# Kernel optimization log

Hardware: AMD Instinct MI355X
Metric: run time of the kernel (lower is better)

The kernel has to match this reference:

```python
import jax, jax.numpy as jnp
import numpy as np

DIM, HEADS, RANK = 768, 12, 64
HEAD_DIM = DIM // HEADS

def _xavier(key, shape):
    fan_in, fan_out = shape[1], shape[0]
    std = (2.0 / (fan_in + fan_out)) ** 0.5
    return std * jax.random.normal(key, shape, dtype=jnp.float32)

def setup_inputs() -> dict:
    key = jax.random.key(0)
    ks = jax.random.split(key, 12)
    B, N = 8, 1024
    x = jax.random.normal(ks[0], (B, N, DIM), dtype=jnp.float32)
    params = {}
    for i, nm in enumerate(['Q', 'K', 'V']):
        params[f'W_{nm}0'] = _xavier(ks[1 + 3 * i], (DIM, RANK))
        params[f'W_{nm}1'] = _xavier(ks[2 + 3 * i], (HEADS, RANK))
        params[f'W_{nm}2'] = _xavier(ks[3 + 3 * i], (HEAD_DIM, RANK))
    proj_w = _xavier(ks[10], (DIM, DIM))
    proj_b = jnp.zeros((DIM,), dtype=jnp.float32)
    return dict(x=x, W_Q0=params['W_Q0'], W_Q1=params['W_Q1'], W_Q2=params['W_Q2'],
                W_K0=params['W_K0'], W_K1=params['W_K1'], W_K2=params['W_K2'],
                W_V0=params['W_V0'], W_V1=params['W_V1'], W_V2=params['W_V2'],
                proj_w=proj_w, proj_b=proj_b)

def _cp_proj(xh, W2, W1, W0, B, N, H, hd):
    # xh: [B,N,H,hd]; contract head_dim with W2 and heads with W1 -> [B,N,R], then expand to dim via W0
    t = jnp.einsum('blnd,dr,nr->blr', xh, W2, W1)
    out = jnp.einsum('blr,mr->blm', t, W0)          # [B,N,dim]
    return out.reshape(B, N, H, hd).transpose(0, 2, 1, 3)  # [B,H,N,hd]

def reference(x, W_Q0, W_Q1, W_Q2, W_K0, W_K1, W_K2, W_V0, W_V1, W_V2, proj_w, proj_b):
    B, N, C = x.shape
    H = W_Q1.shape[0]
    hd = C // H
    scale = hd ** -0.5
    xh = x.reshape(B, N, H, hd)
    q = _cp_proj(xh, W_Q2, W_Q1, W_Q0, B, N, H, hd)
    k = _cp_proj(xh, W_K2, W_K1, W_K0, B, N, H, hd)
    v = _cp_proj(xh, W_V2, W_V1, W_V0, B, N, H, hd)
    attn = jax.nn.softmax(jnp.einsum('bhqd,bhkd->bhqk', q, k) * scale, axis=-1)
    out = jnp.einsum('bhqk,bhkd->bhqd', attn, v).transpose(0, 2, 1, 3).reshape(B, N, C)
    return out @ proj_w.T + proj_b
```

## Files before the change

### kernel.cpp

```cpp
#include <hip/hip_runtime.h>

typedef unsigned short u16;
typedef __attribute__((ext_vector_type(8))) short bf16x8;
typedef __attribute__((ext_vector_type(4))) float f32x4;
typedef __attribute__((ext_vector_type(4))) unsigned short u16x4;

#define AS1 __attribute__((address_space(1)))
#define AS3 __attribute__((address_space(3)))

__device__ __forceinline__ float b2f(u16 s) {
    return __uint_as_float(((unsigned)s) << 16);
}
__device__ __forceinline__ u16 f2b(float f) {
    unsigned u = __float_as_uint(f);
    unsigned r = 0x7fffu + ((u >> 16) & 1u);
    return (u16)((u + r) >> 16);
}

__device__ __forceinline__ void g2l16(const u16* g, u16* l) {
    __builtin_amdgcn_global_load_lds((const AS1 void*)g, (AS3 void*)l, 16, 0, 0);
}

#if __has_builtin(__builtin_amdgcn_exp2f)
#define EXP2(x) __builtin_amdgcn_exp2f(x)
#else
#define EXP2(x) exp2f(x)
#endif

__global__ __launch_bounds__(256) void cast_f32_bf16(
    const float* __restrict__ s, u16* __restrict__ d, int n4)
{
    const int i = blockIdx.x * 256 + threadIdx.x;
    if (i < n4) {
        const float4 v = ((const float4*)s)[i];
        u16x4 o;
        o.x = f2b(v.x); o.y = f2b(v.y); o.z = f2b(v.z); o.w = f2b(v.w);
        ((u16x4*)d)[i] = o;
    }
}

__global__ __launch_bounds__(256) void build_small(
    const float* __restrict__ Wq0, const float* __restrict__ Wq1, const float* __restrict__ Wq2,
    const float* __restrict__ Wk0, const float* __restrict__ Wk1, const float* __restrict__ Wk2,
    const float* __restrict__ Wv0, const float* __restrict__ Wv1, const float* __restrict__ Wv2,
    u16* __restrict__ G, u16* __restrict__ W0b)
{
    const int idx = blockIdx.x * 256 + threadIdx.x;
    if (idx < 147456) {
        const int row = idx / 768, c = idx - row * 768;
        const int which = row >> 6, r = row & 63;
        const int h = c >> 6, d = c & 63;
        const float* W1 = (which == 0) ? Wq1 : (which == 1) ? Wk1 : Wv1;
        const float* W2 = (which == 0) ? Wq2 : (which == 1) ? Wk2 : Wv2;
        G[idx] = f2b(W1[h * 64 + r] * W2[d * 64 + r]);
    } else {
        const int j = idx - 147456;
        const int row = j >> 6, r = j & 63;
        const int which = row / 768, mm = row - which * 768;
        const float* W0 = (which == 0) ? Wq0 : (which == 1) ? Wk0 : Wv0;
        const float scale = (which == 0) ? 0.125f * 1.4426950408889634f : 1.0f;
        W0b[j] = f2b(W0[mm * 64 + r] * scale);
    }
}

__global__ __launch_bounds__(256, 2) void gemm_t(
    const u16* __restrict__ A, const u16* __restrict__ G, u16* __restrict__ T)
{
    __shared__ u16 As[64 * 32];
    __shared__ u16 Bs[64 * 32];

    const int tid = threadIdx.x;
    const int lane = tid & 63, wv = tid >> 6;
    const int l15 = lane & 15, quad = lane >> 4;
    const int rowBase = blockIdx.y * 64;
    const int colBase = blockIdx.x * 64;

    const int srow = wv * 16 + (lane >> 2);
    const int scol = (lane & 3) * 8;
    const u16* aSrc = A + (size_t)(rowBase + srow) * 768 + scol;
    const u16* bSrc = G + (size_t)(colBase + srow) * 768 + scol;
    u16* aDst = As + wv * 512;
    u16* bDst = Bs + wv * 512;

    const f32x4 zero4 = {0.f, 0.f, 0.f, 0.f};
    f32x4 acc[4];
#pragma unroll
    for (int tn = 0; tn < 4; ++tn) acc[tn] = zero4;

    for (int kk = 0; kk < 768; kk += 32) {
        __syncthreads();
        g2l16(aSrc + kk, aDst);
        g2l16(bSrc + kk, bDst);
        __syncthreads();

        const bf16x8 af = *(const bf16x8*)(As + (wv * 16 + l15) * 32 + quad * 8);
#pragma unroll
        for (int tn = 0; tn < 4; ++tn) {
            const bf16x8 bf = *(const bf16x8*)(Bs + (tn * 16 + l15) * 32 + quad * 8);
            acc[tn] = __builtin_amdgcn_mfma_f32_16x16x32_bf16(af, bf, acc[tn], 0, 0, 0);
        }
    }

#pragma unroll
    for (int tn = 0; tn < 4; ++tn) {
        const int col = colBase + tn * 16 + l15;
#pragma unroll
        for (int r = 0; r < 4; ++r) {
            const int grow = rowBase + wv * 16 + quad * 4 + r;
            T[(size_t)grow * 192 + col] = f2b(acc[tn][r]);
        }
    }
}

__global__ __launch_bounds__(256, 2) void gemm_expand(
    const u16* __restrict__ T, const u16* __restrict__ W0b, u16* __restrict__ qkvp)
{
    __shared__ u16 As[128 * 32];
    __shared__ u16 Bs[128 * 32];

    const int tid  = threadIdx.x;
    const int lane = tid & 63, wv = tid >> 6;
    const int l15  = lane & 15, quad = lane >> 4;
    const int rowBase = blockIdx.y * 128;
    const int colBase = blockIdx.x * 128;
    const int which = blockIdx.x / 6;

    const int srow = wv * 32 + (lane >> 2);
    const int scol = (lane & 3) * 8;
    const u16* aSrc = T   + (size_t)(rowBase + srow) * 192 + which * 64 + scol;
    const u16* bSrc = W0b + (size_t)(colBase + srow) * 64 + scol;
    u16* aDst = As + wv * 1024;
    u16* bDst = Bs + wv * 1024;

    const f32x4 zero4 = {0.f, 0.f, 0.f, 0.f};
    f32x4 acc[4][4];
#pragma unroll
    for (int tm = 0; tm < 4; ++tm)
#pragma unroll
        for (int tn = 0; tn < 4; ++tn) acc[tm][tn] = zero4;

    const int wr = (wv >> 1) * 64, wc = (wv & 1) * 64;

    for (int kk = 0; kk < 64; kk += 32) {
        __syncthreads();
        g2l16(aSrc + kk,           aDst);
        g2l16(aSrc + kk + 16 * 192, aDst + 512);
        g2l16(bSrc + kk,           bDst);
        g2l16(bSrc + kk + 16 * 64,  bDst + 512);
        __syncthreads();

        bf16x8 af[4], bfm[4];
#pragma unroll
        for (int t = 0; t < 4; ++t) {
            af[t]  = *(const bf16x8*)(As + (wr + t * 16 + l15) * 32 + quad * 8);
            bfm[t] = *(const bf16x8*)(Bs + (wc + t * 16 + l15) * 32 + quad * 8);
        }
#pragma unroll
        for (int tm = 0; tm < 4; ++tm)
#pragma unroll
            for (int tn = 0; tn < 4; ++tn)
                acc[tm][tn] = __builtin_amdgcn_mfma_f32_16x16x32_bf16(
                    af[tm], bfm[tn], acc[tm][tn], 0, 0, 0);
    }

    const int mmBase = colBase - which * 768 + wc;
    if (which < 2) {
        u16* outp = qkvp + (size_t)which * 6291456;
#pragma unroll
        for (int tm = 0; tm < 4; ++tm) {
            const int grow = rowBase + wr + tm * 16 + quad * 4;
            const int b = grow >> 10, l = grow & 1023;
#pragma unroll
            for (int tn = 0; tn < 4; ++tn) {
                const int mmv = mmBase + tn * 16 + l15;
                const int h = mmv >> 6, d = mmv & 63;
                const size_t base = (((size_t)(b * 12 + h) * 1024 + l) << 6) + d;
#pragma unroll
                for (int r = 0; r < 4; ++r)
                    outp[base + (size_t)r * 64] = f2b(acc[tm][tn][r]);
            }
        }
    } else {
        u16* outp = qkvp + (size_t)2 * 6291456;
#pragma unroll
        for (int tm = 0; tm < 4; ++tm) {
            const int grow = rowBase + wr + tm * 16 + quad * 4;
            const int b = grow >> 10, l = grow & 1023;
#pragma unroll
            for (int tn = 0; tn < 4; ++tn) {
                const int mmv = mmBase + tn * 16 + l15;
                const int h = mmv >> 6, d = mmv & 63;
                u16x4 pk;
                pk.x = f2b(acc[tm][tn][0]); pk.y = f2b(acc[tm][tn][1]);
                pk.z = f2b(acc[tm][tn][2]); pk.w = f2b(acc[tm][tn][3]);
                *(u16x4*)(outp + (((size_t)(b * 12 + h) * 64 + d) << 10) + l) = pk;
            }
        }
    }
}

__global__ __launch_bounds__(256, 5) void flash_attn4(
    const u16* __restrict__ qkv, u16* __restrict__ o)
{
    const int qt = blockIdx.x;
    const int bh = blockIdx.y;
    const int b = bh / 12, h = bh - b * 12;
    const u16* qp = qkv + (size_t)bh * 65536 + qt * 4096;
    const u16* kp = qkv + 6291456 + (size_t)bh * 65536;
    const u16* vp = qkv + 2 * 6291456 + (size_t)bh * 65536;

    __shared__ u16 Ks[64][72];
    __shared__ u16 Vs[64][72];

    const int t = threadIdx.x;
    const int lane = t & 63, wv = t >> 6;
    const int l15 = lane & 15, quad = lane >> 4;

    bf16x8 qf[2];
    qf[0] = *(const bf16x8*)(qp + (wv * 16 + l15) * 64 + quad * 8);
    qf[1] = *(const bf16x8*)(qp + (wv * 16 + l15) * 64 + 32 + quad * 8);

    const int srow = t >> 2;
    const int scol = (t & 3) * 16;
    const int p5 = srow & 31;
    const int lrow = (srow & 32) | ((p5 & 4) << 2) | ((p5 & 16) >> 1)
                   | ((p5 & 8) >> 1) | (p5 & 3);

    int4 kr0 = *(const int4*)(kp + srow * 64 + scol);
    int4 kr1 = *(const int4*)(kp + srow * 64 + scol + 8);
    int4 vr0 = *(const int4*)(vp + srow * 1024 + scol);
    int4 vr1 = *(const int4*)(vp + srow * 1024 + scol + 8);

    const f32x4 zero4 = {0.f, 0.f, 0.f, 0.f};
    f32x4 o_acc[4];
    float l_sum = 0.f;
#pragma unroll
    for (int tn = 0; tn < 4; ++tn) o_acc[tn] = zero4;

    for (int kt = 0; kt < 16; ++kt) {
        __syncthreads();
        *(int4*)&Ks[lrow][scol]     = kr0;
        *(int4*)&Ks[lrow][scol + 8] = kr1;
        *(int4*)&Vs[srow][scol]     = vr0;
        *(int4*)&Vs[srow][scol + 8] = vr1;
        __syncthreads();

        if (kt < 15) {
            kr0 = *(const int4*)(kp + (kt + 1) * 4096 + srow * 64 + scol);
            kr1 = *(const int4*)(kp + (kt + 1) * 4096 + srow * 64 + scol + 8);
            vr0 = *(const int4*)(vp + srow * 1024 + (kt + 1) * 64 + scol);
            vr1 = *(const int4*)(vp + srow * 1024 + (kt + 1) * 64 + scol + 8);
        }

        f32x4 Sacc[4];
#pragma unroll
        for (int tk = 0; tk < 4; ++tk) Sacc[tk] = zero4;
#pragma unroll
        for (int ks = 0; ks < 2; ++ks) {
#pragma unroll
            for (int tk = 0; tk < 4; ++tk) {
                const bf16x8 kf = *(const bf16x8*)&Ks[tk * 16 + l15][ks * 32 + quad * 8];
                Sacc[tk] = __builtin_amdgcn_mfma_f32_16x16x32_bf16(kf, qf[ks], Sacc[tk], 0, 0, 0);
            }
        }

        bf16x8 pf8[2] = {};
#pragma unroll
        for (int tk = 0; tk < 4; ++tk) {
            const int g = tk >> 1, hf = (tk & 1) * 4;
            const float p0 = EXP2(Sacc[tk][0]);
            const float p1 = EXP2(Sacc[tk][1]);
            const float p2 = EXP2(Sacc[tk][2]);
            const float p3 = EXP2(Sacc[tk][3]);
            l_sum += (p0 + p1) + (p2 + p3);
            pf8[g][hf + 0] = (short)f2b(p0);
            pf8[g][hf + 1] = (short)f2b(p1);
            pf8[g][hf + 2] = (short)f2b(p2);
            pf8[g][hf + 3] = (short)f2b(p3);
        }

#pragma unroll
        for (int g = 0; g < 2; ++g) {
#pragma unroll
            for (int tn = 0; tn < 4; ++tn) {
                const bf16x8 vf = *(const bf16x8*)&Vs[tn * 16 + l15][g * 32 + quad * 8];
                o_acc[tn] = __builtin_amdgcn_mfma_f32_16x16x32_bf16(pf8[g], vf, o_acc[tn], 0, 0, 0);
            }
        }
    }

    l_sum += __shfl_xor(l_sum, 16, 64);
    l_sum += __shfl_xor(l_sum, 32, 64);

#pragma unroll
    for (int r = 0; r < 4; ++r) {
        const float Lv = __shfl(l_sum, quad * 4 + r, 64);
        const float inv = 1.0f / Lv;
        const int token = qt * 64 + wv * 16 + quad * 4 + r;
#pragma unroll
        for (int tn = 0; tn < 4; ++tn) {
            const int col = h * 64 + tn * 16 + l15;
            o[(size_t)(b * 1024 + token) * 768 + col] = f2b(o_acc[tn][r] * inv);
        }
    }
}

__global__ __launch_bounds__(256, 2) void gemm_proj(
    const u16* __restrict__ A, const u16* __restrict__ Bt,
    float* __restrict__ C, const float* __restrict__ bias)
{
    __shared__ u16 As[128 * 32];
    __shared__ u16 Bs[128 * 32];

    const int tid  = threadIdx.x;
    const int lane = tid & 63, wv = tid >> 6;
    const int l15  = lane & 15, quad = lane >> 4;
    const int rowBase = blockIdx.y * 128;
    const int colBase = blockIdx.x * 128;

    const int srow = wv * 32 + (lane >> 2);
    const int scol = (lane & 3) * 8;
    const u16* aSrc = A  + (size_t)(rowBase + srow) * 768 + scol;
    const u16* bSrc = Bt + (size_t)(colBase + srow) * 768 + scol;
    u16* aDst = As + wv * 1024;
    u16* bDst = Bs + wv * 1024;

    const f32x4 zero4 = {0.f, 0.f, 0.f, 0.f};
    f32x4 acc[4][4];
#pragma unroll
    for (int tm = 0; tm < 4; ++tm)
#pragma unroll
        for (int tn = 0; tn < 4; ++tn) acc[tm][tn] = zero4;

    const int wr = (wv >> 1) * 64, wc = (wv & 1) * 64;

    for (int kk = 0; kk < 768; kk += 32) {
        __syncthreads();
        g2l16(aSrc + kk,            aDst);
        g2l16(aSrc + kk + 16 * 768, aDst + 512);
        g2l16(bSrc + kk,            bDst);
        g2l16(bSrc + kk + 16 * 768, bDst + 512);
        __syncthreads();

        bf16x8 af[4], bfm[4];
#pragma unroll
        for (int t = 0; t < 4; ++t) {
            af[t]  = *(const bf16x8*)(As + (wr + t * 16 + l15) * 32 + quad * 8);
            bfm[t] = *(const bf16x8*)(Bs + (wc + t * 16 + l15) * 32 + quad * 8);
        }
#pragma unroll
        for (int tm = 0; tm < 4; ++tm)
#pragma unroll
            for (int tn = 0; tn < 4; ++tn)
                acc[tm][tn] = __builtin_amdgcn_mfma_f32_16x16x32_bf16(
                    af[tm], bfm[tn], acc[tm][tn], 0, 0, 0);
    }

#pragma unroll
    for (int tm = 0; tm < 4; ++tm) {
        const int grow = rowBase + wr + tm * 16 + quad * 4;
#pragma unroll
        for (int tn = 0; tn < 4; ++tn) {
            const int gcol = colBase + wc + tn * 16 + l15;
            const float bv = bias[gcol];
#pragma unroll
            for (int r = 0; r < 4; ++r)
                C[(size_t)(grow + r) * 768 + gcol] = acc[tm][tn][r] + bv;
        }
    }
}

extern "C" void kernel_launch(void* const* d_in, const int* in_sizes, int n_in,
                              void* d_out, int out_size, void* d_ws, size_t ws_size,
                              hipStream_t stream)
{
    const float* x      = (const float*)d_in[0];
    const float* Wq0    = (const float*)d_in[1];
    const float* Wq1    = (const float*)d_in[2];
    const float* Wq2    = (const float*)d_in[3];
    const float* Wk0    = (const float*)d_in[4];
    const float* Wk1    = (const float*)d_in[5];
    const float* Wk2    = (const float*)d_in[6];
    const float* Wv0    = (const float*)d_in[7];
    const float* Wv1    = (const float*)d_in[8];
    const float* Wv2    = (const float*)d_in[9];
    const float* proj_w = (const float*)d_in[10];
    const float* proj_b = (const float*)d_in[11];
    float* outp = (float*)d_out;

    char* ws = (char*)d_ws;
    u16* T    = (u16*)ws;
    u16* G    = (u16*)(ws + 3145728);
    u16* W0b  = (u16*)(ws + 3440640);
    u16* pwb  = (u16*)(ws + 3145728);
    u16* xb   = (u16*)(ws + 4325376);
    u16* attn = xb;
    u16* qkv  = (u16*)(ws + 16908288);

    cast_f32_bf16<<<6144, 256, 0, stream>>>(x, xb, 1572864);
    build_small<<<1152, 256, 0, stream>>>(Wq0, Wq1, Wq2, Wk0, Wk1, Wk2, Wv0, Wv1, Wv2, G, W0b);
    gemm_t<<<dim3(3, 128), 256, 0, stream>>>(xb, G, T);
    gemm_expand<<<dim3(18, 64), 256, 0, stream>>>(T, W0b, qkv);
    cast_f32_bf16<<<576, 256, 0, stream>>>(proj_w, pwb, 147456);
    flash_attn4<<<dim3(16, 96), 256, 0, stream>>>(qkv, attn);
    gemm_proj<<<dim3(6, 64), 256, 0, stream>>>(attn, pwb, outp, proj_b);
}
```

Baseline: 192.9 us.

## Fuse input casts into GEMM and weight builder; widen flash attention tile

The separate cast kernel for x is removed. gemm_t now loads fp32 x directly, converts it to bf16 in registers and stores it to LDS, with a register prefetch of the next k-slice. The proj_w cast is folded into build_small, which cuts two kernel launches and the bf16 round trip of x through memory. Flash attention now handles 128 queries per block (two 16-row groups per wave) so K/V tiles are reused twice. It computes the row sum with an MFMA against a ones vector and packs P by truncation instead of round-to-nearest. Occupancy drops (launch bounds 5 to 3), and the truncated P adds slight numeric bias.

```diff
diff --git a/kernel.cpp b/kernel.cpp
--- a/kernel.cpp
+++ b/kernel.cpp
@@ -4,6 +4,7 @@
 typedef __attribute__((ext_vector_type(8))) short bf16x8;
 typedef __attribute__((ext_vector_type(4))) float f32x4;
 typedef __attribute__((ext_vector_type(4))) unsigned short u16x4;
+typedef __attribute__((ext_vector_type(8))) unsigned short u16x8;
 
 #define AS1 __attribute__((address_space(1)))
 #define AS3 __attribute__((address_space(3)))
@@ -15,6 +16,14 @@
     unsigned u = __float_as_uint(f);
     unsigned r = 0x7fffu + ((u >> 16) & 1u);
     return (u16)((u + r) >> 16);
+}
+
+__device__ __forceinline__ unsigned packtrunc(float p0, float p1) {
+#if __has_builtin(__builtin_amdgcn_perm)
+    return __builtin_amdgcn_perm(__float_as_uint(p1), __float_as_uint(p0), 0x07060302u);
+#else
+    return (__float_as_uint(p0) >> 16) | (__float_as_uint(p1) & 0xffff0000u);
+#endif
 }
 
 __device__ __forceinline__ void g2l16(const u16* g, u16* l) {
@@ -27,23 +36,12 @@
 #define EXP2(x) exp2f(x)
 #endif
 
-__global__ __launch_bounds__(256) void cast_f32_bf16(
-    const float* __restrict__ s, u16* __restrict__ d, int n4)
-{
-    const int i = blockIdx.x * 256 + threadIdx.x;
-    if (i < n4) {
-        const float4 v = ((const float4*)s)[i];
-        u16x4 o;
-        o.x = f2b(v.x); o.y = f2b(v.y); o.z = f2b(v.z); o.w = f2b(v.w);
-        ((u16x4*)d)[i] = o;
-    }
-}
-
 __global__ __launch_bounds__(256) void build_small(
     const float* __restrict__ Wq0, const float* __restrict__ Wq1, const float* __restrict__ Wq2,
     const float* __restrict__ Wk0, const float* __restrict__ Wk1, const float* __restrict__ Wk2,
     const float* __restrict__ Wv0, const float* __restrict__ Wv1, const float* __restrict__ Wv2,
-    u16* __restrict__ G, u16* __restrict__ W0b)
+    const float* __restrict__ PW,
+    u16* __restrict__ G, u16* __restrict__ W0b, u16* __restrict__ pwb)
 {
     const int idx = blockIdx.x * 256 + threadIdx.x;
     if (idx < 147456) {
@@ -53,18 +51,24 @@
         const float* W1 = (which == 0) ? Wq1 : (which == 1) ? Wk1 : Wv1;
         const float* W2 = (which == 0) ? Wq2 : (which == 1) ? Wk2 : Wv2;
         G[idx] = f2b(W1[h * 64 + r] * W2[d * 64 + r]);
-    } else {
+    } else if (idx < 294912) {
         const int j = idx - 147456;
         const int row = j >> 6, r = j & 63;
         const int which = row / 768, mm = row - which * 768;
         const float* W0 = (which == 0) ? Wq0 : (which == 1) ? Wk0 : Wv0;
         const float scale = (which == 0) ? 0.125f * 1.4426950408889634f : 1.0f;
         W0b[j] = f2b(W0[mm * 64 + r] * scale);
+    } else {
+        const int j = idx - 294912;
+        const float4 v = ((const float4*)PW)[j];
+        u16x4 o;
+        o.x = f2b(v.x); o.y = f2b(v.y); o.z = f2b(v.z); o.w = f2b(v.w);
+        ((u16x4*)pwb)[j] = o;
     }
 }
 
 __global__ __launch_bounds__(256, 2) void gemm_t(
-    const u16* __restrict__ A, const u16* __restrict__ G, u16* __restrict__ T)
+    const float* __restrict__ X, const u16* __restrict__ G, u16* __restrict__ T)
 {
     __shared__ u16 As[64 * 32];
     __shared__ u16 Bs[64 * 32];
@@ -75,12 +79,14 @@
     const int rowBase = blockIdx.y * 64;
     const int colBase = blockIdx.x * 64;
 
-    const int srow = wv * 16 + (lane >> 2);
-    const int scol = (lane & 3) * 8;
-    const u16* aSrc = A + (size_t)(rowBase + srow) * 768 + scol;
-    const u16* bSrc = G + (size_t)(colBase + srow) * 768 + scol;
-    u16* aDst = As + wv * 512;
-    u16* bDst = Bs + wv * 512;
+    const int srow = tid >> 2;
+    const int scol = (tid & 3) * 8;
+    const float* aS = X + (size_t)(rowBase + srow) * 768 + scol;
+    const u16*  bS  = G + (size_t)(colBase + srow) * 768 + scol;
+
+    float4 a0 = *(const float4*)(aS);
+    float4 a1 = *(const float4*)(aS + 4);
+    int4   b0 = *(const int4*)(bS);
 
     const f32x4 zero4 = {0.f, 0.f, 0.f, 0.f};
     f32x4 acc[4];
@@ -89,9 +95,18 @@
 
     for (int kk = 0; kk < 768; kk += 32) {
         __syncthreads();
-        g2l16(aSrc + kk, aDst);
-        g2l16(bSrc + kk, bDst);
-        __syncthreads();
+        u16x8 ap;
+        ap[0] = f2b(a0.x); ap[1] = f2b(a0.y); ap[2] = f2b(a0.z); ap[3] = f2b(a0.w);
+        ap[4] = f2b(a1.x); ap[5] = f2b(a1.y); ap[6] = f2b(a1.z); ap[7] = f2b(a1.w);
+        *(u16x8*)&As[srow * 32 + scol] = ap;
+        *(int4*)&Bs[srow * 32 + scol]  = b0;
+        __syncthreads();
+
+        if (kk < 736) {
+            a0 = *(const float4*)(aS + kk + 32);
+            a1 = *(const float4*)(aS + kk + 36);
+            b0 = *(const int4*)(bS + kk + 32);
+        }
 
         const bf16x8 af = *(const bf16x8*)(As + (wv * 16 + l15) * 32 + quad * 8);
 #pragma unroll
@@ -143,9 +158,9 @@
 
     for (int kk = 0; kk < 64; kk += 32) {
         __syncthreads();
-        g2l16(aSrc + kk,           aDst);
+        g2l16(aSrc + kk,            aDst);
         g2l16(aSrc + kk + 16 * 192, aDst + 512);
-        g2l16(bSrc + kk,           bDst);
+        g2l16(bSrc + kk,            bDst);
         g2l16(bSrc + kk + 16 * 64,  bDst + 512);
         __syncthreads();
 
@@ -199,13 +214,13 @@
     }
 }
 
-__global__ __launch_bounds__(256, 5) void flash_attn4(
+__global__ __launch_bounds__(256, 3) void flash_attn5(
     const u16* __restrict__ qkv, u16* __restrict__ o)
 {
     const int qt = blockIdx.x;
     const int bh = blockIdx.y;
     const int b = bh / 12, h = bh - b * 12;
-    const u16* qp = qkv + (size_t)bh * 65536 + qt * 4096;
+    const u16* qp = qkv + (size_t)bh * 65536 + qt * 8192;
     const u16* kp = qkv + 6291456 + (size_t)bh * 65536;
     const u16* vp = qkv + 2 * 6291456 + (size_t)bh * 65536;
 
@@ -216,9 +231,12 @@
     const int lane = t & 63, wv = t >> 6;
     const int l15 = lane & 15, quad = lane >> 4;
 
-    bf16x8 qf[2];
-    qf[0] = *(const bf16x8*)(qp + (wv * 16 + l15) * 64 + quad * 8);
-    qf[1] = *(const bf16x8*)(qp + (wv * 16 + l15) * 64 + 32 + quad * 8);
+    bf16x8 qf[2][2];
+#pragma unroll
+    for (int qg = 0; qg < 2; ++qg) {
+        qf[qg][0] = *(const bf16x8*)(qp + (wv * 32 + qg * 16 + l15) * 64 + quad * 8);
+        qf[qg][1] = *(const bf16x8*)(qp + (wv * 32 + qg * 16 + l15) * 64 + 32 + quad * 8);
+    }
 
     const int srow = t >> 2;
     const int scol = (t & 3) * 16;
@@ -226,16 +244,24 @@
     const int lrow = (srow & 32) | ((p5 & 4) << 2) | ((p5 & 16) >> 1)
                    | ((p5 & 8) >> 1) | (p5 & 3);
 
+    bf16x8 vone = {};
+    if (l15 == 0) {
+#pragma unroll
+        for (int j = 0; j < 8; ++j) vone[j] = (short)0x3F80;
+    }
+
     int4 kr0 = *(const int4*)(kp + srow * 64 + scol);
     int4 kr1 = *(const int4*)(kp + srow * 64 + scol + 8);
     int4 vr0 = *(const int4*)(vp + srow * 1024 + scol);
     int4 vr1 = *(const int4*)(vp + srow * 1024 + scol + 8);
 
     const f32x4 zero4 = {0.f, 0.f, 0.f, 0.f};
-    f32x4 o_acc[4];
-    float l_sum = 0.f;
-#pragma unroll
-    for (int tn = 0; tn < 4; ++tn) o_acc[tn] = zero4;
+    f32x4 o_acc[2][4];
+    f32x4 Lacc[2] = {zero4, zero4};
+#pragma unroll
+    for (int qg = 0; qg < 2; ++qg)
+#pragma unroll
+        for (int tn = 0; tn < 4; ++tn) o_acc[qg][tn] = zero4;
 
     for (int kt = 0; kt < 16; ++kt) {
         __syncthreads();
@@ -252,55 +278,60 @@
             vr1 = *(const int4*)(vp + srow * 1024 + (kt + 1) * 64 + scol + 8);
         }
 
-        f32x4 Sacc[4];
-#pragma unroll
-        for (int tk = 0; tk < 4; ++tk) Sacc[tk] = zero4;
+        f32x4 Sacc[2][4];
+#pragma unroll
+        for (int qg = 0; qg < 2; ++qg)
+#pragma unroll
+            for (int tk = 0; tk < 4; ++tk) Sacc[qg][tk] = zero4;
 #pragma unroll
         for (int ks = 0; ks < 2; ++ks) {
 #pragma unroll
             for (int tk = 0; tk < 4; ++tk) {
                 const bf16x8 kf = *(const bf16x8*)&Ks[tk * 16 + l15][ks * 32 + quad * 8];
-                Sacc[tk] = __builtin_amdgcn_mfma_f32_16x16x32_bf16(kf, qf[ks], Sacc[tk], 0, 0, 0);
-            }
-        }
-
-        bf16x8 pf8[2] = {};
-#pragma unroll
-        for (int tk = 0; tk < 4; ++tk) {
-            const int g = tk >> 1, hf = (tk & 1) * 4;
-            const float p0 = EXP2(Sacc[tk][0]);
-            const float p1 = EXP2(Sacc[tk][1]);
-            const float p2 = EXP2(Sacc[tk][2]);
-            const float p3 = EXP2(Sacc[tk][3]);
-            l_sum += (p0 + p1) + (p2 + p3);
-            pf8[g][hf + 0] = (short)f2b(p0);
-            pf8[g][hf + 1] = (short)f2b(p1);
-            pf8[g][hf + 2] = (short)f2b(p2);
-            pf8[g][hf + 3] = (short)f2b(p3);
-        }
+                Sacc[0][tk] = __builtin_amdgcn_mfma_f32_16x16x32_bf16(kf, qf[0][ks], Sacc[0][tk], 0, 0, 0);
+                Sacc[1][tk] = __builtin_amdgcn_mfma_f32_16x16x32_bf16(kf, qf[1][ks], Sacc[1][tk], 0, 0, 0);
+            }
+        }
+
+        union { bf16x8 v; unsigned u[4]; } pf[2][2];
+#pragma unroll
+        for (int qg = 0; qg < 2; ++qg)
+#pragma unroll
+            for (int tk = 0; tk < 4; ++tk) {
+                const float p0 = EXP2(Sacc[qg][tk][0]);
+                const float p1 = EXP2(Sacc[qg][tk][1]);
+                const float p2 = EXP2(Sacc[qg][tk][2]);
+                const float p3 = EXP2(Sacc[qg][tk][3]);
+                const int g = tk >> 1, hf = (tk & 1) * 2;
+                pf[qg][g].u[hf + 0] = packtrunc(p0, p1);
+                pf[qg][g].u[hf + 1] = packtrunc(p2, p3);
+            }
 
 #pragma unroll
         for (int g = 0; g < 2; ++g) {
 #pragma unroll
             for (int tn = 0; tn < 4; ++tn) {
                 const bf16x8 vf = *(const bf16x8*)&Vs[tn * 16 + l15][g * 32 + quad * 8];
-                o_acc[tn] = __builtin_amdgcn_mfma_f32_16x16x32_bf16(pf8[g], vf, o_acc[tn], 0, 0, 0);
-            }
-        }
-    }
-
-    l_sum += __shfl_xor(l_sum, 16, 64);
-    l_sum += __shfl_xor(l_sum, 32, 64);
-
-#pragma unroll
-    for (int r = 0; r < 4; ++r) {
-        const float Lv = __shfl(l_sum, quad * 4 + r, 64);
-        const float inv = 1.0f / Lv;
-        const int token = qt * 64 + wv * 16 + quad * 4 + r;
-#pragma unroll
-        for (int tn = 0; tn < 4; ++tn) {
-            const int col = h * 64 + tn * 16 + l15;
-            o[(size_t)(b * 1024 + token) * 768 + col] = f2b(o_acc[tn][r] * inv);
+                o_acc[0][tn] = __builtin_amdgcn_mfma_f32_16x16x32_bf16(pf[0][g].v, vf, o_acc[0][tn], 0, 0, 0);
+                o_acc[1][tn] = __builtin_amdgcn_mfma_f32_16x16x32_bf16(pf[1][g].v, vf, o_acc[1][tn], 0, 0, 0);
+            }
+            Lacc[0] = __builtin_amdgcn_mfma_f32_16x16x32_bf16(pf[0][g].v, vone, Lacc[0], 0, 0, 0);
+            Lacc[1] = __builtin_amdgcn_mfma_f32_16x16x32_bf16(pf[1][g].v, vone, Lacc[1], 0, 0, 0);
+        }
+    }
+
+#pragma unroll
+    for (int qg = 0; qg < 2; ++qg) {
+#pragma unroll
+        for (int r = 0; r < 4; ++r) {
+            const float Lv = __shfl(Lacc[qg][r], quad << 4, 64);
+            const float inv = 1.0f / Lv;
+            const int token = qt * 128 + wv * 32 + qg * 16 + quad * 4 + r;
+#pragma unroll
+            for (int tn = 0; tn < 4; ++tn) {
+                const int col = h * 64 + tn * 16 + l15;
+                o[(size_t)(b * 1024 + token) * 768 + col] = f2b(o_acc[qg][tn][r] * inv);
+            }
         }
     }
 }
@@ -392,16 +423,14 @@
     u16* T    = (u16*)ws;
     u16* G    = (u16*)(ws + 3145728);
     u16* W0b  = (u16*)(ws + 3440640);
-    u16* pwb  = (u16*)(ws + 3145728);
-    u16* xb   = (u16*)(ws + 4325376);
-    u16* attn = xb;
-    u16* qkv  = (u16*)(ws + 16908288);
-
-    cast_f32_bf16<<<6144, 256, 0, stream>>>(x, xb, 1572864);
-    build_small<<<1152, 256, 0, stream>>>(Wq0, Wq1, Wq2, Wk0, Wk1, Wk2, Wv0, Wv1, Wv2, G, W0b);
-    gemm_t<<<dim3(3, 128), 256, 0, stream>>>(xb, G, T);
+    u16* pwb  = (u16*)(ws + 3735552);
+    u16* attn = (u16*)(ws + 4915200);
+    u16* qkv  = (u16*)(ws + 17498112);
+
+    build_small<<<1728, 256, 0, stream>>>(Wq0, Wq1, Wq2, Wk0, Wk1, Wk2, Wv0, Wv1, Wv2,
+                                          proj_w, G, W0b, pwb);
+    gemm_t<<<dim3(3, 128), 256, 0, stream>>>(x, G, T);
     gemm_expand<<<dim3(18, 64), 256, 0, stream>>>(T, W0b, qkv);
-    cast_f32_bf16<<<576, 256, 0, stream>>>(proj_w, pwb, 147456);
-    flash_attn4<<<dim3(16, 96), 256, 0, stream>>>(qkv, attn);
+    flash_attn5<<<dim3(8, 96), 256, 0, stream>>>(qkv, attn);
     gemm_proj<<<dim3(6, 64), 256, 0, stream>>>(attn, pwb, outp, proj_b);
 }
```

New measurement: 185.9 us. -3.6%, faster.
